# Optimization experiments

Hardware: AMD Instinct MI355X
Metric: run time of the kernel (lower is better)

## Reference

```python
import jax, jax.numpy as jnp
import numpy as np

D_MODEL = 1024
D_STATE = 16
D_CONV = 4
EXPAND = 2
D_INNER = EXPAND * D_MODEL  # 2048
BATCH = 2
SEQ = 2048


def setup_inputs() -> dict:
    key = jax.random.key(0)
    ks = jax.random.split(key, 7)
    s = 0.02
    x = jax.random.normal(ks[0], (BATCH, SEQ, D_MODEL), jnp.float32)
    in_proj_w = jax.random.normal(ks[1], (2 * D_INNER, D_MODEL), jnp.float32) * s
    conv_w = jax.random.normal(ks[2], (D_INNER, 1, D_CONV), jnp.float32) * s  # depthwise: groups=d_inner
    conv_b = jnp.zeros((D_INNER,), jnp.float32)
    x_proj_w = jax.random.normal(ks[3], (2 * D_STATE, D_INNER), jnp.float32) * s
    dt_proj_w = jax.random.normal(ks[4], (D_INNER, D_INNER), jnp.float32) * s
    dt_proj_b = jnp.zeros((D_INNER,), jnp.float32)
    # A = arange(1..d_state) repeated for each inner channel; A_log = log(A)
    A_log = jnp.log(jnp.tile(jnp.arange(1, D_STATE + 1, dtype=jnp.float32), (D_INNER, 1)))
    D_param = jnp.ones((D_INNER,), jnp.float32)
    out_proj_w = jax.random.normal(ks[5], (D_MODEL, D_INNER), jnp.float32) * s
    return {"x": x, "in_proj_w": in_proj_w, "conv_w": conv_w, "conv_b": conv_b,
            "x_proj_w": x_proj_w, "dt_proj_w": dt_proj_w, "dt_proj_b": dt_proj_b,
            "A_log": A_log, "D_param": D_param, "out_proj_w": out_proj_w}


def reference(x, in_proj_w, conv_w, conv_b, x_proj_w, dt_proj_w, dt_proj_b, A_log, D_param, out_proj_w):
    B, L, _ = x.shape
    # input projection -> [B, L, 2*d_inner], split into ssm path and gate
    xz = x @ in_proj_w.T
    x_ssm, z = jnp.split(xz, 2, axis=-1)

    # causal depthwise conv1d (torch pads both sides by d_conv-1 then slices [:L])
    xc = jnp.transpose(x_ssm, (0, 2, 1))  # [B, d_inner, L]
    xc = jnp.pad(xc, ((0, 0), (0, 0), (D_CONV - 1, 0)))
    xc = jax.lax.conv_general_dilated(
        xc, conv_w, window_strides=(1,), padding='VALID',
        dimension_numbers=('NCH', 'OIH', 'NCH'), feature_group_count=D_INNER)
    xc = xc + conv_b[None, :, None]
    x_act = jax.nn.silu(jnp.transpose(xc, (0, 2, 1)))  # [B, L, d_inner]

    delta = jax.nn.softplus(x_act @ dt_proj_w.T + dt_proj_b)  # [B, L, d_inner]
    bc = x_act @ x_proj_w.T                                   # [B, L, 2*d_state]
    B_p, C_p = jnp.split(bc, 2, axis=-1)

    A = -jnp.exp(A_log)  # [d_inner, d_state]

    def step(h, inp):
        u_i, d_i, B_i, C_i = inp  # [B,d], [B,d], [B,n], [B,n]
        dA = jnp.exp(d_i[..., None] * A)                       # [B, d, n]
        h = dA * h + (d_i * u_i)[..., None] * B_i[:, None, :]  # [B, d, n]
        y = jnp.einsum('bdn,bn->bd', h, C_i)
        return h, y

    h0 = jnp.zeros((B, D_INNER, D_STATE), x.dtype)
    seq = (jnp.swapaxes(x_act, 0, 1), jnp.swapaxes(delta, 0, 1),
           jnp.swapaxes(B_p, 0, 1), jnp.swapaxes(C_p, 0, 1))
    _, ys = jax.lax.scan(step, h0, seq)  # ys: [L, B, d_inner]
    y_ssm = jnp.swapaxes(ys, 0, 1) + x_act * D_param

    y = y_ssm * jax.nn.silu(z)
    return y @ out_proj_w.T
```

## Files before the change

### kernel.cpp

```cpp
#include <hip/hip_runtime.h>
#include <hip/hip_bf16.h>
#include <math.h>

#define DM 1024
#define DS 16
#define DI 2048
#define NB 2
#define LL 2048
#define BL (NB*LL)
#define LC 32
#define NC (LL/LC)

typedef __attribute__((ext_vector_type(8))) short short8;
typedef __attribute__((ext_vector_type(8))) unsigned short ushort8;
typedef __attribute__((ext_vector_type(4))) float f32x4;

__device__ __forceinline__ float silu_f(float x){ return x / (1.f + __expf(-x)); }
__device__ __forceinline__ float softplus_f(float x){ return (x > 15.f) ? x : log1pf(__expf(x)); }
__device__ __forceinline__ unsigned short f2bf(float f){
  unsigned u = __float_as_uint(f);
  u += 0x7fff + ((u >> 16) & 1);
  return (unsigned short)(u >> 16);
}
__device__ __forceinline__ float bf2f(unsigned short v){
  return __uint_as_float(((unsigned)v) << 16);
}

__global__ __launch_bounds__(256) void f2b_k(const float* __restrict__ src,
                                             unsigned short* __restrict__ dst, int n)
{
  int i = (blockIdx.x * 256 + threadIdx.x) * 8;
  if (i >= n) return;
  float4 v0 = *(const float4*)&src[i];
  float4 v1 = *(const float4*)&src[i + 4];
  ushort8 o;
  o[0]=f2bf(v0.x); o[1]=f2bf(v0.y); o[2]=f2bf(v0.z); o[3]=f2bf(v0.w);
  o[4]=f2bf(v1.x); o[5]=f2bf(v1.y); o[6]=f2bf(v1.z); o[7]=f2bf(v1.w);
  *(ushort8*)&dst[i] = o;
}

__global__ __launch_bounds__(256) void f2b_multi(
    const float* __restrict__ s0, unsigned short* __restrict__ d0, int c0,
    const float* __restrict__ s1, unsigned short* __restrict__ d1, int c1,
    const float* __restrict__ s2, unsigned short* __restrict__ d2, int c2,
    const float* __restrict__ s3, unsigned short* __restrict__ d3, int c3)
{
  int b = blockIdx.x;
  const float* s; unsigned short* d;
  if (b < c0)              { s = s0; d = d0; }
  else if ((b -= c0) < c1) { s = s1; d = d1; }
  else if ((b -= c1) < c2) { s = s2; d = d2; }
  else                     { b -= c2; s = s3; d = d3; }
  int i = (b * 256 + threadIdx.x) * 8;
  float4 v0 = *(const float4*)&s[i];
  float4 v1 = *(const float4*)&s[i + 4];
  ushort8 o;
  o[0]=f2bf(v0.x); o[1]=f2bf(v0.y); o[2]=f2bf(v0.z); o[3]=f2bf(v0.w);
  o[4]=f2bf(v1.x); o[5]=f2bf(v1.y); o[6]=f2bf(v1.z); o[7]=f2bf(v1.w);
  *(ushort8*)&d[i] = o;
}

template<int BN, int WAVESN, int EPI, int OUTBF>
__global__ __launch_bounds__(512, 2) void gemm3(
    const unsigned short* __restrict__ A, const unsigned short* __restrict__ Bw,
    const float* __restrict__ bias, void* __restrict__ Cp,
    int M, int N, int K)
{
  constexpr int BM = 256;
  constexpr int WM = BM / (8 / WAVESN);
  constexpr int WN = BN / WAVESN;
  constexpr int MR = WM / 16;
  constexpr int NRJ = WN / 16;
  constexpr int SLOADS = 4 + BN / 64;
  __shared__ unsigned short lds[2][(BM + BN) * 64];
  const int t = threadIdx.x;
  const int wid = t >> 6, lane = t & 63;
  const int nbx = N / BN;
  const int cpx = (nbx * (M / BM)) >> 3;
  const int bid = (int)blockIdx.x;
  const int swz = (bid & 7) * cpx + (bid >> 3);
  const int bm = (swz / nbx) * BM, bn = (swz % nbx) * BN;
  const int wm = (wid / WAVESN) * WM, wn = (wid % WAVESN) * WN;
  const int srow8 = lane >> 3;
  const int sch   = lane & 7;

  f32x4 acc[MR][NRJ] = {};

  auto stage = [&](int buf, int kt) {
    const int k0 = kt * 64;
    #pragma unroll
    for (int p = 0; p < 4; p++) {
      int row = p * 64 + wid * 8 + srow8;
      int ch = sch ^ (row & 7);
      __builtin_amdgcn_global_load_lds(
        (const __attribute__((address_space(1))) void*)(A + (size_t)(bm + row) * K + k0 + ch * 8),
        (__attribute__((address_space(3))) void*)(&lds[buf][(p * 64 + wid * 8) * 64]), 16, 0, 0);
    }
    #pragma unroll
    for (int p = 0; p < BN / 64; p++) {
      int row = p * 64 + wid * 8 + srow8;
      int ch = sch ^ (row & 7);
      __builtin_amdgcn_global_load_lds(
        (const __attribute__((address_space(1))) void*)(Bw + (size_t)(bn + row) * K + k0 + ch * 8),
        (__attribute__((address_space(3))) void*)(&lds[buf][(BM + p * 64 + wid * 8) * 64]), 16, 0, 0);
    }
  };

  const int nk = K / 64;
  stage(0, 0);
  stage(1, 1);
  asm volatile("s_waitcnt vmcnt(%0)" :: "n"(SLOADS) : "memory");
  __builtin_amdgcn_s_barrier();

  int cur = 0;
  for (int kt = 0; kt < nk; kt++) {
    const unsigned short* bufA = &lds[cur][0];
    const unsigned short* bufB = &lds[cur][BM * 64];
    #pragma unroll
    for (int ks = 0; ks < 2; ks++) {
      short8 af[MR], bfr[NRJ];
      #pragma unroll
      for (int i = 0; i < MR; i++) {
        int r = wm + i * 16 + (lane & 15);
        int c = ((ks << 2) + (lane >> 4)) ^ (r & 7);
        af[i] = *(const short8*)&bufA[r * 64 + c * 8];
      }
      #pragma unroll
      for (int j = 0; j < NRJ; j++) {
        int r = wn + j * 16 + (lane & 15);
        int c = ((ks << 2) + (lane >> 4)) ^ (r & 7);
        bfr[j] = *(const short8*)&bufB[r * 64 + c * 8];
      }
      #pragma unroll
      for (int i = 0; i < MR; i++)
        #pragma unroll
        for (int j = 0; j < NRJ; j++)
          acc[i][j] = __builtin_amdgcn_mfma_f32_16x16x32_bf16(af[i], bfr[j], acc[i][j], 0, 0, 0);
    }
    if (kt < nk - 2) {
      __builtin_amdgcn_s_barrier();
      stage(cur, kt + 2);
      asm volatile("s_waitcnt vmcnt(%0)" :: "n"(SLOADS) : "memory");
      __builtin_amdgcn_s_barrier();
    } else if (kt == nk - 2) {
      asm volatile("s_waitcnt vmcnt(0)" ::: "memory");
      __builtin_amdgcn_s_barrier();
    }
    cur ^= 1;
  }

  #pragma unroll
  for (int i = 0; i < MR; i++) {
    #pragma unroll
    for (int j = 0; j < NRJ; j++) {
      int col = bn + wn + j * 16 + (lane & 15);
      float bv = (EPI == 1) ? bias[col] : 0.f;
      #pragma unroll
      for (int r = 0; r < 4; r++) {
        int row = bm + wm + i * 16 + (lane >> 4) * 4 + r;
        float v = acc[i][j][r];
        if (EPI == 1) v = softplus_f(v + bv);
        if (OUTBF) ((unsigned short*)Cp)[(size_t)row * N + col] = f2bf(v);
        else       ((float*)Cp)[(size_t)row * N + col] = v;
      }
    }
  }
}

__global__ __launch_bounds__(256) void conv_silu_k(
    const unsigned short* __restrict__ xz, const float* __restrict__ cw,
    const float* __restrict__ cb, unsigned short* __restrict__ xa)
{
  int v = blockIdx.x * 256 + threadIdx.x;
  int d8 = (v & (DI/8 - 1)) * 8;
  int bl = v >> 8;
  int l  = bl & (LL - 1);
  float acc[8];
  #pragma unroll
  for (int j = 0; j < 8; j++) acc[j] = cb[d8 + j];
  size_t rowb = (size_t)bl * (2 * DI) + d8;
  #pragma unroll
  for (int k = 0; k < 4; k++) {
    int ls = l - 3 + k;
    if (ls >= 0) {
      ushort8 xv = *(const ushort8*)&xz[rowb + (size_t)(k - 3) * (2 * DI)];
      #pragma unroll
      for (int j = 0; j < 8; j++) acc[j] += bf2f(xv[j]) * cw[(d8 + j) * 4 + k];
    }
  }
  ushort8 o;
  #pragma unroll
  for (int j = 0; j < 8; j++) o[j] = f2bf(silu_f(acc[j]));
  *(ushort8*)&xa[(size_t)bl * DI + d8] = o;
}

__global__ __launch_bounds__(256) void bc_k(
    const unsigned short* __restrict__ xa, const unsigned short* __restrict__ w,
    float* __restrict__ bc)
{
  __shared__ unsigned short sx[8 * DI];
  const int t = threadIdx.x;
  const size_t base = (size_t)blockIdx.x * 8 * DI;
  #pragma unroll
  for (int it = 0; it < 8; it++) {
    int v = t + it * 256;
    *(ushort8*)&sx[v * 8] = *(const ushort8*)&xa[base + (size_t)v * 8];
  }
  __syncthreads();
  const int m = t >> 5, n = t & 31;
  const unsigned short* wr = w + (size_t)n * DI;
  const unsigned short* xr = sx + m * DI;
  float acc = 0.f;
  #pragma unroll 4
  for (int k = 0; k < DI; k += 8) {
    ushort8 xv = *(const ushort8*)&xr[k];
    ushort8 wv = *(const ushort8*)&wr[k];
    #pragma unroll
    for (int j = 0; j < 8; j++) acc += bf2f(xv[j]) * bf2f(wv[j]);
  }
  bc[(size_t)(blockIdx.x * 8 + m) * 32 + n] = acc;
}

__global__ __launch_bounds__(256) void scan_part1(
    const float* __restrict__ dlt, const unsigned short* __restrict__ xa,
    const float* __restrict__ bc, const float* __restrict__ A_log,
    float* __restrict__ S_arr, float* __restrict__ sumdlt)
{
  const int bid = blockIdx.x;
  const int b = bid >> 9;
  const int c = (bid >> 3) & (NC - 1);
  const int dg = bid & 7;
  const int t = threadIdx.x;
  const int d = dg * 256 + t;
  float Ac[16];
  #pragma unroll
  for (int n = 0; n < 16; n++) Ac[n] = -__expf(A_log[d * 16 + n]);
  __shared__ float sB[LC][16];
  for (int e = t; e < LC * 16; e += 256) {
    int l = e >> 4, n = e & 15;
    sB[l][n] = bc[(size_t)(b * LL + c * LC + l) * 32 + n];
  }
  __syncthreads();
  float h[16] = {};
  float sd = 0.f;
  size_t rowbase = (size_t)(b * LL + c * LC) * DI + d;
  for (int l = 0; l < LC; l++) {
    float dl = dlt[rowbase + (size_t)l * DI];
    float u  = bf2f(xa[rowbase + (size_t)l * DI]);
    float w = dl * u;
    sd += dl;
    #pragma unroll
    for (int n = 0; n < 16; n++) {
      float dA = __expf(dl * Ac[n]);
      h[n] = dA * h[n] + w * sB[l][n];
    }
  }
  float* Sp = S_arr + ((size_t)(b * NC + c) * DI + d) * 16;
  #pragma unroll
  for (int n = 0; n < 16; n++) Sp[n] = h[n];
  sumdlt[(size_t)(b * NC + c) * DI + d] = sd;
}

__global__ __launch_bounds__(256) void scan_combine(
    const float* __restrict__ A_log, const float* __restrict__ sumdlt,
    float* __restrict__ S_arr)
{
  int tid = blockIdx.x * 256 + threadIdx.x;
  int n = tid & 15;
  int d = (tid >> 4) & (DI - 1);
  int b = tid >> 15;
  float Ac = -__expf(A_log[d * 16 + n]);
  float h = 0.f;
  for (int c = 0; c < NC; c++) {
    size_t idx = ((size_t)(b * NC + c) * DI + d) * 16 + n;
    float S = S_arr[idx];
    float P = __expf(sumdlt[(size_t)(b * NC + c) * DI + d] * Ac);
    S_arr[idx] = h;
    h = P * h + S;
  }
}

__global__ __launch_bounds__(256) void scan_part2(
    const float* __restrict__ dlt, const unsigned short* __restrict__ xa,
    const float* __restrict__ bc, const float* __restrict__ A_log,
    const float* __restrict__ Dp, const unsigned short* __restrict__ xz,
    const float* __restrict__ Hin, unsigned short* __restrict__ y)
{
  const int bid = blockIdx.x;
  const int b = bid >> 9;
  const int c = (bid >> 3) & (NC - 1);
  const int dg = bid & 7;
  const int t = threadIdx.x;
  const int d = dg * 256 + t;
  float Ac[16];
  #pragma unroll
  for (int n = 0; n < 16; n++) Ac[n] = -__expf(A_log[d * 16 + n]);
  __shared__ float sB[LC][16];
  __shared__ float sC[LC][16];
  for (int e = t; e < LC * 16; e += 256) {
    int l = e >> 4, n = e & 15;
    size_t row = (size_t)(b * LL + c * LC + l) * 32;
    sB[l][n] = bc[row + n];
    sC[l][n] = bc[row + 16 + n];
  }
  __syncthreads();
  float h[16];
  const float* Hp = Hin + ((size_t)(b * NC + c) * DI + d) * 16;
  #pragma unroll
  for (int n = 0; n < 16; n++) h[n] = Hp[n];
  const float Dv = Dp[d];
  size_t rowbase = (size_t)(b * LL + c * LC) * DI + d;
  for (int l = 0; l < LC; l++) {
    float dl = dlt[rowbase + (size_t)l * DI];
    float u  = bf2f(xa[rowbase + (size_t)l * DI]);
    float w = dl * u;
    float ya = 0.f;
    #pragma unroll
    for (int n = 0; n < 16; n++) {
      float dA = __expf(dl * Ac[n]);
      h[n] = dA * h[n] + w * sB[l][n];
      ya += h[n] * sC[l][n];
    }
    float zz = bf2f(xz[(size_t)(b * LL + c * LC + l) * (2 * DI) + DI + d]);
    y[rowbase + (size_t)l * DI] = f2bf((ya + u * Dv) * silu_f(zz));
  }
}

extern "C" void kernel_launch(void* const* d_in, const int* in_sizes, int n_in,
                              void* d_out, int out_size, void* d_ws, size_t ws_size,
                              hipStream_t stream)
{
  const float* x    = (const float*)d_in[0];
  const float* Win  = (const float*)d_in[1];
  const float* cw   = (const float*)d_in[2];
  const float* cb   = (const float*)d_in[3];
  const float* Wxp  = (const float*)d_in[4];
  const float* Wdt  = (const float*)d_in[5];
  const float* bdt  = (const float*)d_in[6];
  const float* Alog = (const float*)d_in[7];
  const float* Dp   = (const float*)d_in[8];
  const float* Wout = (const float*)d_in[9];
  float* out = (float*)d_out;

  float* ws = (float*)d_ws;
  float* dlt    = ws;
  float* bcb    = dlt + 8388608;
  float* S_arr  = bcb + 131072;
  float* sumdlt = S_arr + 4194304;
  unsigned short* xz_bf = (unsigned short*)(sumdlt + 262144);
  unsigned short* xa_bf = xz_bf + 16777216;
  unsigned short* y_bf  = xa_bf + 8388608;
  unsigned short* x_bf  = y_bf;
  unsigned short* win_bf= y_bf + 4194304;
  unsigned short* wbuf  = y_bf + 8388608;
  unsigned short* wxp_bf= wbuf + 4194304;

  f2b_multi<<<dim3(2048 + 2048 + 2048 + 32), dim3(256), 0, stream>>>(
      x, x_bf, 2048, Win, win_bf, 2048, Wdt, wbuf, 2048, Wxp, wxp_bf, 32);
  gemm3<256,4,0,1><<<dim3(256), dim3(512), 0, stream>>>(x_bf, win_bf, nullptr, xz_bf, BL, 2*DI, DM);
  conv_silu_k<<<dim3(BL*DI/8/256), dim3(256), 0, stream>>>(xz_bf, cw, cb, xa_bf);
  gemm3<128,2,1,0><<<dim3(256), dim3(512), 0, stream>>>(xa_bf, wbuf, bdt, dlt, BL, DI, DI);
  f2b_k<<<dim3(DM*DI/2048), dim3(256), 0, stream>>>(Wout, wbuf, DM*DI);
  bc_k<<<dim3(BL/8), dim3(256), 0, stream>>>(xa_bf, wxp_bf, bcb);
  scan_part1<<<dim3(NB*NC*8), dim3(256), 0, stream>>>(dlt, xa_bf, bcb, Alog, S_arr, sumdlt);
  scan_combine<<<dim3(NB*DI*DS/256), dim3(256), 0, stream>>>(Alog, sumdlt, S_arr);
  scan_part2<<<dim3(NB*NC*8), dim3(256), 0, stream>>>(dlt, xa_bf, bcb, Alog, Dp, xz_bf, S_arr, y_bf);
  gemm3<64,2,0,0><<<dim3(256), dim3(512), 0, stream>>>(y_bf, wbuf, nullptr, out, BL, DM, DI);
}
```

Baseline: 346.5 us.

## Store delta and scan chunk states in bf16, simplify GEMM pipeline

Delta from the dt-projection GEMM is now written as bf16 instead of fp32, and the per-chunk scan states and carries are kept in bf16 with vectorized loads and stores. This roughly halves the memory traffic for these intermediates across the scan kernels. The GEMM is replaced by a simpler variant with a fixed 2x4 wave layout (128 rows per wave) and a single-stage prefetch with __syncthreads, which drops the deeper two-ahead vmcnt-based pipelining. Keeping the scan state and delta in bf16 costs precision in a long recurrence, and the simpler GEMM may hide memory latency less well.

```diff
diff --git a/kernel.cpp b/kernel.cpp
--- a/kernel.cpp
+++ b/kernel.cpp
@@ -60,18 +60,14 @@
   *(ushort8*)&d[i] = o;
 }
 
-template<int BN, int WAVESN, int EPI, int OUTBF>
-__global__ __launch_bounds__(512, 2) void gemm3(
+template<int BN, int EPI, int OUTBF>
+__global__ __launch_bounds__(512, 2) void gemm2(
     const unsigned short* __restrict__ A, const unsigned short* __restrict__ Bw,
     const float* __restrict__ bias, void* __restrict__ Cp,
     int M, int N, int K)
 {
   constexpr int BM = 256;
-  constexpr int WM = BM / (8 / WAVESN);
-  constexpr int WN = BN / WAVESN;
-  constexpr int MR = WM / 16;
-  constexpr int NRJ = WN / 16;
-  constexpr int SLOADS = 4 + BN / 64;
+  constexpr int NR = BN / 64;
   __shared__ unsigned short lds[2][(BM + BN) * 64];
   const int t = threadIdx.x;
   const int wid = t >> 6, lane = t & 63;
@@ -80,16 +76,15 @@
   const int bid = (int)blockIdx.x;
   const int swz = (bid & 7) * cpx + (bid >> 3);
   const int bm = (swz / nbx) * BM, bn = (swz % nbx) * BN;
-  const int wm = (wid / WAVESN) * WM, wn = (wid % WAVESN) * WN;
+  const int wm = (wid >> 2) * 128, wn = (wid & 3) * (BN / 4);
   const int srow8 = lane >> 3;
   const int sch   = lane & 7;
 
-  f32x4 acc[MR][NRJ] = {};
-
-  auto stage = [&](int buf, int kt) {
-    const int k0 = kt * 64;
-    #pragma unroll
-    for (int p = 0; p < 4; p++) {
+  f32x4 acc[8][NR] = {};
+
+  auto stage = [&](int buf, int k0) {
+    #pragma unroll
+    for (int p = 0; p < BM / 64; p++) {
       int row = p * 64 + wid * 8 + srow8;
       int ch = sch ^ (row & 7);
       __builtin_amdgcn_global_load_lds(
@@ -106,53 +101,42 @@
     }
   };
 
+  stage(0, 0);
+  __syncthreads();
   const int nk = K / 64;
-  stage(0, 0);
-  stage(1, 1);
-  asm volatile("s_waitcnt vmcnt(%0)" :: "n"(SLOADS) : "memory");
-  __builtin_amdgcn_s_barrier();
-
   int cur = 0;
   for (int kt = 0; kt < nk; kt++) {
+    if (kt + 1 < nk) stage(cur ^ 1, (kt + 1) * 64);
     const unsigned short* bufA = &lds[cur][0];
     const unsigned short* bufB = &lds[cur][BM * 64];
     #pragma unroll
     for (int ks = 0; ks < 2; ks++) {
-      short8 af[MR], bfr[NRJ];
-      #pragma unroll
-      for (int i = 0; i < MR; i++) {
+      short8 af[8], bfr[NR];
+      #pragma unroll
+      for (int i = 0; i < 8; i++) {
         int r = wm + i * 16 + (lane & 15);
         int c = ((ks << 2) + (lane >> 4)) ^ (r & 7);
         af[i] = *(const short8*)&bufA[r * 64 + c * 8];
       }
       #pragma unroll
-      for (int j = 0; j < NRJ; j++) {
+      for (int j = 0; j < NR; j++) {
         int r = wn + j * 16 + (lane & 15);
         int c = ((ks << 2) + (lane >> 4)) ^ (r & 7);
         bfr[j] = *(const short8*)&bufB[r * 64 + c * 8];
       }
       #pragma unroll
-      for (int i = 0; i < MR; i++)
+      for (int i = 0; i < 8; i++)
         #pragma unroll
-        for (int j = 0; j < NRJ; j++)
+        for (int j = 0; j < NR; j++)
           acc[i][j] = __builtin_amdgcn_mfma_f32_16x16x32_bf16(af[i], bfr[j], acc[i][j], 0, 0, 0);
     }
-    if (kt < nk - 2) {
-      __builtin_amdgcn_s_barrier();
-      stage(cur, kt + 2);
-      asm volatile("s_waitcnt vmcnt(%0)" :: "n"(SLOADS) : "memory");
-      __builtin_amdgcn_s_barrier();
-    } else if (kt == nk - 2) {
-      asm volatile("s_waitcnt vmcnt(0)" ::: "memory");
-      __builtin_amdgcn_s_barrier();
-    }
+    __syncthreads();
     cur ^= 1;
   }
-
-  #pragma unroll
-  for (int i = 0; i < MR; i++) {
-    #pragma unroll
-    for (int j = 0; j < NRJ; j++) {
+  #pragma unroll
+  for (int i = 0; i < 8; i++) {
+    #pragma unroll
+    for (int j = 0; j < NR; j++) {
       int col = bn + wn + j * 16 + (lane & 15);
       float bv = (EPI == 1) ? bias[col] : 0.f;
       #pragma unroll
@@ -222,9 +206,9 @@
 }
 
 __global__ __launch_bounds__(256) void scan_part1(
-    const float* __restrict__ dlt, const unsigned short* __restrict__ xa,
+    const unsigned short* __restrict__ dlt, const unsigned short* __restrict__ xa,
     const float* __restrict__ bc, const float* __restrict__ A_log,
-    float* __restrict__ S_arr, float* __restrict__ sumdlt)
+    unsigned short* __restrict__ S_bf, float* __restrict__ sumdlt)
 {
   const int bid = blockIdx.x;
   const int b = bid >> 9;
@@ -245,7 +229,7 @@
   float sd = 0.f;
   size_t rowbase = (size_t)(b * LL + c * LC) * DI + d;
   for (int l = 0; l < LC; l++) {
-    float dl = dlt[rowbase + (size_t)l * DI];
+    float dl = bf2f(dlt[rowbase + (size_t)l * DI]);
     float u  = bf2f(xa[rowbase + (size_t)l * DI]);
     float w = dl * u;
     sd += dl;
@@ -255,15 +239,18 @@
       h[n] = dA * h[n] + w * sB[l][n];
     }
   }
-  float* Sp = S_arr + ((size_t)(b * NC + c) * DI + d) * 16;
-  #pragma unroll
-  for (int n = 0; n < 16; n++) Sp[n] = h[n];
+  unsigned short* Sp = S_bf + ((size_t)(b * NC + c) * DI + d) * 16;
+  ushort8 s0, s1;
+  #pragma unroll
+  for (int n = 0; n < 8; n++) { s0[n] = f2bf(h[n]); s1[n] = f2bf(h[8 + n]); }
+  *(ushort8*)&Sp[0] = s0;
+  *(ushort8*)&Sp[8] = s1;
   sumdlt[(size_t)(b * NC + c) * DI + d] = sd;
 }
 
 __global__ __launch_bounds__(256) void scan_combine(
     const float* __restrict__ A_log, const float* __restrict__ sumdlt,
-    float* __restrict__ S_arr)
+    unsigned short* __restrict__ S_bf)
 {
   int tid = blockIdx.x * 256 + threadIdx.x;
   int n = tid & 15;
@@ -273,18 +260,18 @@
   float h = 0.f;
   for (int c = 0; c < NC; c++) {
     size_t idx = ((size_t)(b * NC + c) * DI + d) * 16 + n;
-    float S = S_arr[idx];
+    float S = bf2f(S_bf[idx]);
     float P = __expf(sumdlt[(size_t)(b * NC + c) * DI + d] * Ac);
-    S_arr[idx] = h;
+    S_bf[idx] = f2bf(h);
     h = P * h + S;
   }
 }
 
 __global__ __launch_bounds__(256) void scan_part2(
-    const float* __restrict__ dlt, const unsigned short* __restrict__ xa,
+    const unsigned short* __restrict__ dlt, const unsigned short* __restrict__ xa,
     const float* __restrict__ bc, const float* __restrict__ A_log,
     const float* __restrict__ Dp, const unsigned short* __restrict__ xz,
-    const float* __restrict__ Hin, unsigned short* __restrict__ y)
+    const unsigned short* __restrict__ Hin, unsigned short* __restrict__ y)
 {
   const int bid = blockIdx.x;
   const int b = bid >> 9;
@@ -305,13 +292,15 @@
   }
   __syncthreads();
   float h[16];
-  const float* Hp = Hin + ((size_t)(b * NC + c) * DI + d) * 16;
-  #pragma unroll
-  for (int n = 0; n < 16; n++) h[n] = Hp[n];
+  const unsigned short* Hp = Hin + ((size_t)(b * NC + c) * DI + d) * 16;
+  ushort8 h0 = *(const ushort8*)&Hp[0];
+  ushort8 h1 = *(const ushort8*)&Hp[8];
+  #pragma unroll
+  for (int n = 0; n < 8; n++) { h[n] = bf2f(h0[n]); h[8 + n] = bf2f(h1[n]); }
   const float Dv = Dp[d];
   size_t rowbase = (size_t)(b * LL + c * LC) * DI + d;
   for (int l = 0; l < LC; l++) {
-    float dl = dlt[rowbase + (size_t)l * DI];
+    float dl = bf2f(dlt[rowbase + (size_t)l * DI]);
     float u  = bf2f(xa[rowbase + (size_t)l * DI]);
     float w = dl * u;
     float ya = 0.f;
@@ -343,10 +332,10 @@
   float* out = (float*)d_out;
 
   float* ws = (float*)d_ws;
-  float* dlt    = ws;
-  float* bcb    = dlt + 8388608;
-  float* S_arr  = bcb + 131072;
-  float* sumdlt = S_arr + 4194304;
+  unsigned short* dlt_bf = (unsigned short*)ws;
+  float* bcb    = ws + 4194304;
+  unsigned short* S_bf = (unsigned short*)(bcb + 131072);
+  float* sumdlt = (float*)(S_bf + 4194304);
   unsigned short* xz_bf = (unsigned short*)(sumdlt + 262144);
   unsigned short* xa_bf = xz_bf + 16777216;
   unsigned short* y_bf  = xa_bf + 8388608;
@@ -357,13 +346,13 @@
 
   f2b_multi<<<dim3(2048 + 2048 + 2048 + 32), dim3(256), 0, stream>>>(
       x, x_bf, 2048, Win, win_bf, 2048, Wdt, wbuf, 2048, Wxp, wxp_bf, 32);
-  gemm3<256,4,0,1><<<dim3(256), dim3(512), 0, stream>>>(x_bf, win_bf, nullptr, xz_bf, BL, 2*DI, DM);
+  gemm2<256,0,1><<<dim3(256), dim3(512), 0, stream>>>(x_bf, win_bf, nullptr, xz_bf, BL, 2*DI, DM);
   conv_silu_k<<<dim3(BL*DI/8/256), dim3(256), 0, stream>>>(xz_bf, cw, cb, xa_bf);
-  gemm3<128,2,1,0><<<dim3(256), dim3(512), 0, stream>>>(xa_bf, wbuf, bdt, dlt, BL, DI, DI);
+  gemm2<128,1,1><<<dim3(256), dim3(512), 0, stream>>>(xa_bf, wbuf, bdt, dlt_bf, BL, DI, DI);
   f2b_k<<<dim3(DM*DI/2048), dim3(256), 0, stream>>>(Wout, wbuf, DM*DI);
   bc_k<<<dim3(BL/8), dim3(256), 0, stream>>>(xa_bf, wxp_bf, bcb);
-  scan_part1<<<dim3(NB*NC*8), dim3(256), 0, stream>>>(dlt, xa_bf, bcb, Alog, S_arr, sumdlt);
-  scan_combine<<<dim3(NB*DI*DS/256), dim3(256), 0, stream>>>(Alog, sumdlt, S_arr);
-  scan_part2<<<dim3(NB*NC*8), dim3(256), 0, stream>>>(dlt, xa_bf, bcb, Alog, Dp, xz_bf, S_arr, y_bf);
-  gemm3<64,2,0,0><<<dim3(256), dim3(512), 0, stream>>>(y_bf, wbuf, nullptr, out, BL, DM, DI);
-}
+  scan_part1<<<dim3(NB*NC*8), dim3(256), 0, stream>>>(dlt_bf, xa_bf, bcb, Alog, S_bf, sumdlt);
+  scan_combine<<<dim3(NB*DI*DS/256), dim3(256), 0, stream>>>(Alog, sumdlt, S_bf);
+  scan_part2<<<dim3(NB*NC*8), dim3(256), 0, stream>>>(dlt_bf, xa_bf, bcb, Alog, Dp, xz_bf, S_bf, y_bf);
+  gemm2<64,0,0><<<dim3(256), dim3(512), 0, stream>>>(y_bf, wbuf, nullptr, out, BL, DM, DI);
+}
```

Measured after the change: 335.4 us. 3.2% less time.
